# Kernel optimization log

Hardware: AMD Instinct MI355X
Metric: run time of the kernel (lower is better)

The kernel has to match this reference:

```python
import jax, jax.numpy as jnp
import numpy as np

B, C, N = 4, 64, 512
H = 128  # hidden width; MLP input is 2*C = 128


def setup_inputs() -> dict:
    key = jax.random.key(0)
    k0, k1, k2 = jax.random.split(key, 3)
    x = jax.random.normal(k0, (B, C, N), dtype=jnp.float32)
    # Torch Linear init ~ U(-1/sqrt(fan_in), 1/sqrt(fan_in)); stored as (in, out) for einsum.
    W1 = jax.random.normal(k1, (2 * C, H), dtype=jnp.float32) * (1.0 / np.sqrt(2 * C))
    b1 = jnp.zeros((H,), dtype=jnp.float32)
    W2 = jax.random.normal(k2, (H, 1), dtype=jnp.float32) * (1.0 / np.sqrt(H))
    b2 = jnp.zeros((1,), dtype=jnp.float32)
    return {"x": x, "W1": W1, "b1": b1, "W2": W2, "b2": b2}


def reference(x, W1, b1, W2, b2):
    # x: (B, C, N). Equivalent to the per-offset loop: for every pair (i, j) with
    # j > i, score = MLP(concat(x[:, :, i], x[:, :, j])), placed at y[:, i, j].
    # Dropout is identity in eval mode.
    b, c, n = x.shape
    xt = jnp.transpose(x, (0, 2, 1))                      # (B, N, C)
    left = jnp.broadcast_to(xt[:, :, None, :], (b, n, n, c))   # row index i
    right = jnp.broadcast_to(xt[:, None, :, :], (b, n, n, c))  # col index j
    pairs = jnp.concatenate([left, right], axis=-1)       # (B, N, N, 2C)
    h = jax.nn.relu(jnp.einsum('bijc,ch->bijh', pairs, W1) + b1)
    score = (jnp.einsum('bijh,ho->bijo', h, W2) + b2)[..., 0]  # (B, N, N)
    mask = jnp.triu(jnp.ones((n, n), dtype=score.dtype), k=1)  # strict upper triangle
    return score * mask
```

## Files before the change

### kernel.cpp

```cpp
#include <hip/hip_runtime.h>

#define B_ 4
#define C_ 64
#define N_ 512
#define H_ 128

__global__ __launch_bounds__(256) void proj_kernel(
    const float* __restrict__ x, const float* __restrict__ W1,
    const float* __restrict__ b1, float* __restrict__ Lbuf,
    float* __restrict__ Rbuf)
{
    __shared__ float Wl[64 * 128];
    __shared__ float xs[16 * 68];

    const int t    = threadIdx.x;
    const int half = blockIdx.x >> 7;
    const int rem  = blockIdx.x & 127;
    const int b    = rem >> 5;
    const int i0   = (rem & 31) * 16;
    const int cbase = half * 64;

    const float4* W14 = (const float4*)W1;
    float4* Wl4 = (float4*)Wl;
    #pragma unroll
    for (int k = 0; k < 8; ++k)
        Wl4[t + k * 256] = W14[cbase * 32 + t + k * 256];

    #pragma unroll
    for (int k = 0; k < 4; ++k) {
        int idx = t + k * 256;
        int c = idx >> 4, ii = idx & 15;
        xs[ii * 68 + c] = x[b * (C_ * N_) + c * N_ + i0 + ii];
    }
    __syncthreads();

    const int hq  = t & 31;
    const int il  = (t >> 5) * 2;
    const int col = hq * 4;

    float4 a0, a1;
    if (half) { a0 = *(const float4*)(b1 + col); a1 = a0; }
    else      { a0 = make_float4(0.f, 0.f, 0.f, 0.f); a1 = a0; }

    #pragma unroll
    for (int c = 0; c < 64; c += 4) {
        float4 xv0 = *(float4*)(xs + il * 68 + c);
        float4 xv1 = *(float4*)(xs + (il + 1) * 68 + c);
        const float* x0p = (const float*)&xv0;
        const float* x1p = (const float*)&xv1;
        #pragma unroll
        for (int cc = 0; cc < 4; ++cc) {
            float4 w = Wl4[(c + cc) * 32 + hq];
            a0.x = fmaf(w.x, x0p[cc], a0.x);
            a0.y = fmaf(w.y, x0p[cc], a0.y);
            a0.z = fmaf(w.z, x0p[cc], a0.z);
            a0.w = fmaf(w.w, x0p[cc], a0.w);
            a1.x = fmaf(w.x, x1p[cc], a1.x);
            a1.y = fmaf(w.y, x1p[cc], a1.y);
            a1.z = fmaf(w.z, x1p[cc], a1.z);
            a1.w = fmaf(w.w, x1p[cc], a1.w);
        }
    }

    float* buf = half ? Rbuf : Lbuf;
    float* o = buf + b * (N_ * H_) + (i0 + il) * H_ + col;
    *(float4*)o = a0;
    *(float4*)(o + H_) = a1;
}

__global__ __launch_bounds__(256) void pair_kernel(
    const float* __restrict__ Lbuf, const float* __restrict__ Rbuf,
    const float* __restrict__ W2, const float* __restrict__ b2,
    float* __restrict__ out)
{
    __shared__ float4 Lt4[32 * 32];
    __shared__ float4 Rt4[32 * 32];

    const int t    = threadIdx.x;
    const int b    = blockIdx.x >> 8;
    const int tile = blockIdx.x & 255;
    const int ti0  = (tile >> 4) * 32;
    const int tj0  = (tile & 15) * 32;

    float* outb = out + b * (N_ * N_);

    if (tj0 + 31 <= ti0) {
        const int r = t >> 3, cq = t & 7;
        *(float4*)(outb + (ti0 + r) * N_ + tj0 + cq * 4) =
            make_float4(0.f, 0.f, 0.f, 0.f);
        return;
    }

    const float* Lsrc = Lbuf + b * (N_ * H_) + ti0 * H_;
    const float* Rsrc = Rbuf + b * (N_ * H_) + tj0 * H_;
    #pragma unroll
    for (int k = 0; k < 4; ++k) {
        int idx = t + k * 256;
        int row = idx >> 5, hc = idx & 31;
        int sc = (hc + (row >> 2)) & 31;
        Lt4[row * 32 + sc] = *(const float4*)(Lsrc + row * H_ + hc * 4);
        Rt4[row * 32 + sc] = *(const float4*)(Rsrc + row * H_ + hc * 4);
    }
    __syncthreads();

    const int w    = t >> 6;
    const int lane = t & 63;
    const int til  = (w >> 1) * 16 + (lane >> 3) * 2;
    const int tjl  = (w & 1) * 16 + (lane & 7) * 2;
    const int rotL = til >> 2;
    const int rotR = tjl >> 2;

    float a00 = 0.f, a01 = 0.f, a10 = 0.f, a11 = 0.f;
    const float4* W24 = (const float4*)W2;

    #pragma unroll 4
    for (int hc = 0; hc < 32; ++hc) {
        float4 L0 = Lt4[til * 32 + ((hc + rotL) & 31)];
        float4 L1 = Lt4[(til + 1) * 32 + ((hc + rotL) & 31)];
        float4 R0 = Rt4[tjl * 32 + ((hc + rotR) & 31)];
        float4 R1 = Rt4[(tjl + 1) * 32 + ((hc + rotR) & 31)];
        float4 wv = W24[hc];
        const float* l0 = (const float*)&L0;
        const float* l1 = (const float*)&L1;
        const float* r0 = (const float*)&R0;
        const float* r1 = (const float*)&R1;
        const float* wp = (const float*)&wv;
        #pragma unroll
        for (int k = 0; k < 4; ++k) {
            a00 = fmaf(fmaxf(l0[k] + r0[k], 0.f), wp[k], a00);
            a01 = fmaf(fmaxf(l0[k] + r1[k], 0.f), wp[k], a01);
            a10 = fmaf(fmaxf(l1[k] + r0[k], 0.f), wp[k], a10);
            a11 = fmaf(fmaxf(l1[k] + r1[k], 0.f), wp[k], a11);
        }
    }

    const float bias2 = b2[0];
    const int gi0 = ti0 + til, gj0 = tj0 + tjl;
    float2 v0, v1;
    v0.x = (gj0     > gi0    ) ? (a00 + bias2) : 0.f;
    v0.y = (gj0 + 1 > gi0    ) ? (a01 + bias2) : 0.f;
    v1.x = (gj0     > gi0 + 1) ? (a10 + bias2) : 0.f;
    v1.y = (gj0 + 1 > gi0 + 1) ? (a11 + bias2) : 0.f;
    *(float2*)(outb + gi0 * N_ + gj0) = v0;
    *(float2*)(outb + (gi0 + 1) * N_ + gj0) = v1;
}

extern "C" void kernel_launch(void* const* d_in, const int* in_sizes, int n_in,
                              void* d_out, int out_size, void* d_ws, size_t ws_size,
                              hipStream_t stream)
{
    const float* x  = (const float*)d_in[0];
    const float* W1 = (const float*)d_in[1];
    const float* b1 = (const float*)d_in[2];
    const float* W2 = (const float*)d_in[3];
    const float* b2 = (const float*)d_in[4];
    float* out  = (float*)d_out;
    float* Lbuf = (float*)d_ws;
    float* Rbuf = Lbuf + B_ * N_ * H_;

    proj_kernel<<<256, 256, 0, stream>>>(x, W1, b1, Lbuf, Rbuf);
    pair_kernel<<<B_ * 256, 256, 0, stream>>>(Lbuf, Rbuf, W2, b2, out);
}
```

Measured before the change: 76.69 us.

## Use packed FP32 math, XOR swizzle, and triangular block ordering

```diff
diff --git a/kernel.cpp b/kernel.cpp
--- a/kernel.cpp
+++ b/kernel.cpp
@@ -4,6 +4,9 @@
 #define C_ 64
 #define N_ 512
 #define H_ 128
+
+typedef float v2f __attribute__((ext_vector_type(2)));
+typedef float v4f __attribute__((ext_vector_type(4)));
 
 __global__ __launch_bounds__(256) void proj_kernel(
     const float* __restrict__ x, const float* __restrict__ W1,
@@ -38,10 +41,15 @@
     const int il  = (t >> 5) * 2;
     const int col = hq * 4;
 
-    float4 a0, a1;
-    if (half) { a0 = *(const float4*)(b1 + col); a1 = a0; }
-    else      { a0 = make_float4(0.f, 0.f, 0.f, 0.f); a1 = a0; }
-
+    v2f a0l = {0.f, 0.f}, a0h = {0.f, 0.f};
+    if (half) {
+        float4 bv = *(const float4*)(b1 + col);
+        a0l = {bv.x, bv.y};
+        a0h = {bv.z, bv.w};
+    }
+    v2f a1l = a0l, a1h = a0h;
+
+    const v4f* Wlv = (const v4f*)Wl;
     #pragma unroll
     for (int c = 0; c < 64; c += 4) {
         float4 xv0 = *(float4*)(xs + il * 68 + c);
@@ -50,22 +58,21 @@
         const float* x1p = (const float*)&xv1;
         #pragma unroll
         for (int cc = 0; cc < 4; ++cc) {
-            float4 w = Wl4[(c + cc) * 32 + hq];
-            a0.x = fmaf(w.x, x0p[cc], a0.x);
-            a0.y = fmaf(w.y, x0p[cc], a0.y);
-            a0.z = fmaf(w.z, x0p[cc], a0.z);
-            a0.w = fmaf(w.w, x0p[cc], a0.w);
-            a1.x = fmaf(w.x, x1p[cc], a1.x);
-            a1.y = fmaf(w.y, x1p[cc], a1.y);
-            a1.z = fmaf(w.z, x1p[cc], a1.z);
-            a1.w = fmaf(w.w, x1p[cc], a1.w);
+            v4f wv = Wlv[(c + cc) * 32 + hq];
+            v2f wl = wv.xy, wh = wv.zw;
+            v2f xb0 = {x0p[cc], x0p[cc]};
+            v2f xb1 = {x1p[cc], x1p[cc]};
+            a0l = __builtin_elementwise_fma(wl, xb0, a0l);
+            a0h = __builtin_elementwise_fma(wh, xb0, a0h);
+            a1l = __builtin_elementwise_fma(wl, xb1, a1l);
+            a1h = __builtin_elementwise_fma(wh, xb1, a1h);
         }
     }
 
     float* buf = half ? Rbuf : Lbuf;
     float* o = buf + b * (N_ * H_) + (i0 + il) * H_ + col;
-    *(float4*)o = a0;
-    *(float4*)(o + H_) = a1;
+    *(float4*)o        = make_float4(a0l.x, a0l.y, a0h.x, a0h.y);
+    *(float4*)(o + H_) = make_float4(a1l.x, a1l.y, a1h.x, a1h.y);
 }
 
 __global__ __launch_bounds__(256) void pair_kernel(
@@ -73,33 +80,44 @@
     const float* __restrict__ W2, const float* __restrict__ b2,
     float* __restrict__ out)
 {
-    __shared__ float4 Lt4[32 * 32];
-    __shared__ float4 Rt4[32 * 32];
-
-    const int t    = threadIdx.x;
-    const int b    = blockIdx.x >> 8;
-    const int tile = blockIdx.x & 255;
-    const int ti0  = (tile >> 4) * 32;
-    const int tj0  = (tile & 15) * 32;
-
+    __shared__ v4f Lt4[32 * 32];
+    __shared__ v4f Rt4[32 * 32];
+
+    const int t = threadIdx.x;
+    int b, it, jt;
+    {
+        int bid = blockIdx.x;
+        if (bid >= 544) {
+            int z = bid - 544;
+            b = z & 3;
+            int k = z >> 2;
+            it = 1;
+            while (k >= it) { k -= it; ++it; }
+            jt = k;
+            float* outb = out + b * (N_ * N_);
+            const int r = t >> 3, cq = t & 7;
+            *(float4*)(outb + (it * 32 + r) * N_ + jt * 32 + cq * 4) =
+                make_float4(0.f, 0.f, 0.f, 0.f);
+            return;
+        }
+        b = bid & 3;
+        int k = bid >> 2;
+        it = 0;
+        while (k >= 16 - it) { k -= 16 - it; ++it; }
+        jt = it + k;
+    }
+    const int ti0 = it * 32, tj0 = jt * 32;
     float* outb = out + b * (N_ * N_);
-
-    if (tj0 + 31 <= ti0) {
-        const int r = t >> 3, cq = t & 7;
-        *(float4*)(outb + (ti0 + r) * N_ + tj0 + cq * 4) =
-            make_float4(0.f, 0.f, 0.f, 0.f);
-        return;
-    }
 
     const float* Lsrc = Lbuf + b * (N_ * H_) + ti0 * H_;
     const float* Rsrc = Rbuf + b * (N_ * H_) + tj0 * H_;
     #pragma unroll
-    for (int k = 0; k < 4; ++k) {
-        int idx = t + k * 256;
+    for (int kk = 0; kk < 4; ++kk) {
+        int idx = t + kk * 256;
         int row = idx >> 5, hc = idx & 31;
-        int sc = (hc + (row >> 2)) & 31;
-        Lt4[row * 32 + sc] = *(const float4*)(Lsrc + row * H_ + hc * 4);
-        Rt4[row * 32 + sc] = *(const float4*)(Rsrc + row * H_ + hc * 4);
+        int sc = hc ^ (row >> 2);
+        Lt4[row * 32 + sc] = *(const v4f*)(Lsrc + row * H_ + hc * 4);
+        Rt4[row * 32 + sc] = *(const v4f*)(Rsrc + row * H_ + hc * 4);
     }
     __syncthreads();
 
@@ -110,31 +128,51 @@
     const int rotL = til >> 2;
     const int rotR = tjl >> 2;
 
-    float a00 = 0.f, a01 = 0.f, a10 = 0.f, a11 = 0.f;
-    const float4* W24 = (const float4*)W2;
-
-    #pragma unroll 4
+    const v4f* Lp  = Lt4 + til * 32;
+    const v4f* Rp  = Rt4 + tjl * 32;
+    const v4f* W24 = (const v4f*)W2;
+
+    v2f c00l = {0.f, 0.f}, c00h = {0.f, 0.f};
+    v2f c01l = {0.f, 0.f}, c01h = {0.f, 0.f};
+    v2f c10l = {0.f, 0.f}, c10h = {0.f, 0.f};
+    v2f c11l = {0.f, 0.f}, c11h = {0.f, 0.f};
+
+    #pragma unroll 8
     for (int hc = 0; hc < 32; ++hc) {
-        float4 L0 = Lt4[til * 32 + ((hc + rotL) & 31)];
-        float4 L1 = Lt4[(til + 1) * 32 + ((hc + rotL) & 31)];
-        float4 R0 = Rt4[tjl * 32 + ((hc + rotR) & 31)];
-        float4 R1 = Rt4[(tjl + 1) * 32 + ((hc + rotR) & 31)];
-        float4 wv = W24[hc];
-        const float* l0 = (const float*)&L0;
-        const float* l1 = (const float*)&L1;
-        const float* r0 = (const float*)&R0;
-        const float* r1 = (const float*)&R1;
-        const float* wp = (const float*)&wv;
-        #pragma unroll
-        for (int k = 0; k < 4; ++k) {
-            a00 = fmaf(fmaxf(l0[k] + r0[k], 0.f), wp[k], a00);
-            a01 = fmaf(fmaxf(l0[k] + r1[k], 0.f), wp[k], a01);
-            a10 = fmaf(fmaxf(l1[k] + r0[k], 0.f), wp[k], a10);
-            a11 = fmaf(fmaxf(l1[k] + r1[k], 0.f), wp[k], a11);
-        }
+        const int oL = hc ^ rotL;
+        const int oR = hc ^ rotR;
+        v4f L0 = Lp[oL];
+        v4f L1 = Lp[32 + oL];
+        v4f R0 = Rp[oR];
+        v4f R1 = Rp[32 + oR];
+        v4f wv = W24[hc];
+        v2f wl = wv.xy, wh = wv.zw;
+        const v2f z2 = {0.f, 0.f};
+        v2f s;
+        s = __builtin_elementwise_max(L0.xy + R0.xy, z2);
+        c00l = __builtin_elementwise_fma(s, wl, c00l);
+        s = __builtin_elementwise_max(L0.zw + R0.zw, z2);
+        c00h = __builtin_elementwise_fma(s, wh, c00h);
+        s = __builtin_elementwise_max(L0.xy + R1.xy, z2);
+        c01l = __builtin_elementwise_fma(s, wl, c01l);
+        s = __builtin_elementwise_max(L0.zw + R1.zw, z2);
+        c01h = __builtin_elementwise_fma(s, wh, c01h);
+        s = __builtin_elementwise_max(L1.xy + R0.xy, z2);
+        c10l = __builtin_elementwise_fma(s, wl, c10l);
+        s = __builtin_elementwise_max(L1.zw + R0.zw, z2);
+        c10h = __builtin_elementwise_fma(s, wh, c10h);
+        s = __builtin_elementwise_max(L1.xy + R1.xy, z2);
+        c11l = __builtin_elementwise_fma(s, wl, c11l);
+        s = __builtin_elementwise_max(L1.zw + R1.zw, z2);
+        c11h = __builtin_elementwise_fma(s, wh, c11h);
     }
 
     const float bias2 = b2[0];
+    float a00 = (c00l.x + c00l.y) + (c00h.x + c00h.y);
+    float a01 = (c01l.x + c01l.y) + (c01h.x + c01h.y);
+    float a10 = (c10l.x + c10l.y) + (c10h.x + c10h.y);
+    float a11 = (c11l.x + c11l.y) + (c11h.x + c11h.y);
+
     const int gi0 = ti0 + til, gj0 = tj0 + tjl;
     float2 v0, v1;
     v0.x = (gj0     > gi0    ) ? (a00 + bias2) : 0.f;
```

After: 75.60 us. About the same (-1.4%).
